# Performance work log

Hardware: AMD Instinct MI355X
Metric: run time of the kernel (lower is better)

Reference implementation:

```python
import jax, jax.numpy as jnp
import numpy as np
from jax import lax

EPS = 1e-8
SLOPE = 0.2

def _modconv(x, wv, W, b, sW, sB, demodulate, pad):
    # StyleGAN2 modulated conv, expressed in the equivalent fused form:
    # scale input by per-sample style s, shared-weight conv, then demodulate output.
    s = wv @ sW.T + sB                                   # [B, Cin]
    y = lax.conv_general_dilated(
        x * s[:, :, None, None], W, (1, 1), [(pad, pad), (pad, pad)],
        dimension_numbers=("NCHW", "OIHW", "NCHW"))      # [B, Cout, H, W]
    if demodulate:
        # d[b,o] = 1/sqrt(sum_{i,k,k} (W[o,i,k,k]*s[b,i])^2 + eps)
        d = lax.rsqrt(jnp.einsum("oihw,bi->bo", W * W, s * s) + EPS)
        y = y * d[:, :, None, None]
    return y + b[None, :, None, None]

def _up2(x):
    B, C, H, W = x.shape
    # matches torch F.interpolate(scale_factor=2, mode='bilinear', align_corners=False)
    return jax.image.resize(x, (B, C, 2 * H, 2 * W), method="bilinear")

def setup_inputs() -> dict:
    B, CIN, COUT, NZ, H = 8, 512, 512, 512, 32
    key = jax.random.key(0)
    ks = jax.random.split(key, 20)
    wscale3 = 1.0 / np.sqrt(CIN * 9)   # kaiming-ish equalized-lr scale baked into weights
    wscale1 = 1.0 / np.sqrt(COUT)
    sscale = 1.0 / np.sqrt(NZ)
    return {
        "maps": jax.random.normal(ks[0], (B, CIN, H, H), jnp.float32),
        "w": jax.random.normal(ks[1], (B, NZ), jnp.float32),
        "rgb": jax.random.normal(ks[2], (B, 3, H, H), jnp.float32),
        "noise0": jax.random.normal(ks[3], (B, 1, 2 * H, 2 * H), jnp.float32),
        "noise1": jax.random.normal(ks[4], (B, 1, 2 * H, 2 * H), jnp.float32),
        "w0": jax.random.normal(ks[5], (COUT, CIN, 3, 3), jnp.float32) * wscale3,
        "b0": jnp.zeros((COUT,), jnp.float32),
        "sW0": jax.random.normal(ks[6], (CIN, NZ), jnp.float32) * sscale,
        "sB0": jnp.ones((CIN,), jnp.float32),
        "ns0": jax.random.normal(ks[7], (COUT,), jnp.float32) * 0.1,
        "w1": jax.random.normal(ks[8], (COUT, COUT, 3, 3), jnp.float32) * wscale3,
        "b1": jnp.zeros((COUT,), jnp.float32),
        "sW1": jax.random.normal(ks[9], (COUT, NZ), jnp.float32) * sscale,
        "sB1": jnp.ones((COUT,), jnp.float32),
        "ns1": jax.random.normal(ks[10], (COUT,), jnp.float32) * 0.1,
        "rgbW": jax.random.normal(ks[11], (3, COUT, 1, 1), jnp.float32) * wscale1,
        "rgbB": jnp.zeros((3,), jnp.float32),
        "rgbSW": jax.random.normal(ks[12], (COUT, NZ), jnp.float32) * sscale,
        "rgbSB": jnp.ones((COUT,), jnp.float32),
    }

def reference(maps, w, rgb, noise0, noise1,
              w0, b0, sW0, sB0, ns0,
              w1, b1, sW1, sB1, ns1,
              rgbW, rgbB, rgbSW, rgbSB):
    rgb = _up2(rgb)
    x = _up2(maps)
    # layer 0: modulated conv 3x3 + noise + leakyrelu
    x = _modconv(x, w, w0, b0, sW0, sB0, True, 1)
    x = x + ns0[None, :, None, None] * noise0
    x = jnp.where(x >= 0, x, SLOPE * x)
    # layer 1
    x = _modconv(x, w, w1, b1, sW1, sB1, True, 1)
    x = x + ns1[None, :, None, None] * noise1
    x = jnp.where(x >= 0, x, SLOPE * x)
    # to_rgb: modulated 1x1 conv, no demodulation
    rgb_out = rgb + _modconv(x, w, rgbW, rgbB, rgbSW, rgbSB, False, 0)
    return (rgb_out, x)
```

## Files before the change

### kernel.cpp

```cpp
#include <hip/hip_runtime.h>

typedef unsigned short u16;
typedef short bf16x8 __attribute__((ext_vector_type(8)));
typedef float f32x4 __attribute__((ext_vector_type(4)));
typedef u16 u16x4 __attribute__((ext_vector_type(4)));
typedef u16 u16x8 __attribute__((ext_vector_type(8)));
typedef unsigned u32x4 __attribute__((ext_vector_type(4)));

__device__ __forceinline__ float b2f(u16 v) {
  union { unsigned u; float f; } x; x.u = ((unsigned)v) << 16; return x.f;
}
__device__ __forceinline__ u16 f2b(float f) {
  unsigned u = __float_as_uint(f);
  unsigned r = (u + 0x7FFFu + ((u >> 16) & 1u)) >> 16;
  return (u16)r;
}
__device__ __forceinline__ float rin(const void* p, size_t i, int bf) {
  return bf ? b2f(((const u16*)p)[i]) : ((const float*)p)[i];
}
__device__ __forceinline__ void async16(const void* g, void* l) {
  __builtin_amdgcn_global_load_lds((const __attribute__((address_space(1))) unsigned*)g,
                                   (__attribute__((address_space(3))) unsigned*)l, 16, 0, 0);
}

__global__ void detect_kernel(const unsigned* __restrict__ w0, int* __restrict__ flag) {
  const int i = threadIdx.x;
  const unsigned lo = w0[i] & 0xFFFFu;
  const unsigned e = (lo >> 7) & 0xFFu;
  const unsigned long long bad = __ballot(e < 100u || e > 126u);
  if (i == 0) flag[0] = (bad == 0ull) ? 1 : 0;
}

__global__ void styleall_kernel(const void* __restrict__ w,
                                const void* __restrict__ sW0, const void* __restrict__ sB0,
                                const void* __restrict__ sW1, const void* __restrict__ sB1,
                                const void* __restrict__ sWR, const void* __restrict__ sBR,
                                float* __restrict__ s0, float* __restrict__ s1,
                                float* __restrict__ sR, const int* __restrict__ flag) {
  const int bf = flag[0];
  const int mat = blockIdx.z, b = blockIdx.y, oc = blockIdx.x;
  const void* sW = (mat == 0) ? sW0 : ((mat == 1) ? sW1 : sWR);
  const void* sB = (mat == 0) ? sB0 : ((mat == 1) ? sB1 : sBR);
  float* out = (mat == 0) ? s0 : ((mat == 1) ? s1 : sR);
  const int tid = threadIdx.x;
  const int i = oc * 64 + (tid >> 2), q = tid & 3;
  float acc = 0.f;
  if (bf) {
    const u16* rp = (const u16*)sW + (size_t)i * 512 + q * 128;
    const u16* wp = (const u16*)w + b * 512 + q * 128;
    for (int z = 0; z < 128; z += 8) {
      u16x8 a = *(const u16x8*)(rp + z), c = *(const u16x8*)(wp + z);
#pragma unroll
      for (int j = 0; j < 8; ++j) acc += b2f(a[j]) * b2f(c[j]);
    }
  } else {
    const float* rp = (const float*)sW + (size_t)i * 512 + q * 128;
    const float* wp = (const float*)w + b * 512 + q * 128;
    for (int z = 0; z < 128; z += 4) {
      f32x4 a = *(const f32x4*)(rp + z), c = *(const f32x4*)(wp + z);
#pragma unroll
      for (int j = 0; j < 4; ++j) acc += a[j] * c[j];
    }
  }
  acc += __shfl_xor(acc, 1, 64);
  acc += __shfl_xor(acc, 2, 64);
  if (q == 0) out[b * 512 + i] = acc + rin(sB, i, bf);
}

__global__ void demod_kernel(const void* __restrict__ W, const float* __restrict__ s,
                             float* __restrict__ d, u16* __restrict__ Wp,
                             const int* __restrict__ flag) {
  const int bf = flag[0];
  const int o = blockIdx.x, tid = threadIdx.x, lane = tid & 63, wv = tid >> 6;
  __shared__ float wsq[512];
  for (int i = tid; i < 512; i += 256) {
    float ss = 0.f;
#pragma unroll
    for (int t = 0; t < 9; ++t) {
      const float f = rin(W, (size_t)(o * 512 + i) * 9 + t, bf);
      ss += f * f;
      Wp[t * 262144 + o * 512 + i] = f2b(f);
    }
    wsq[i] = ss;
  }
  __syncthreads();
#pragma unroll
  for (int bb = 0; bb < 2; ++bb) {
    const int b = wv * 2 + bb;
    float part = 0.f;
    for (int i = lane; i < 512; i += 64) { const float sv = s[b * 512 + i]; part += wsq[i] * sv * sv; }
#pragma unroll
    for (int st = 1; st < 64; st <<= 1) part += __shfl_xor(part, st, 64);
    if (lane == 0) d[b * 512 + o] = rsqrtf(part + 1e-8f);
  }
}

__global__ void upsample_kernel(const void* __restrict__ maps, const float* __restrict__ s,
                                void* __restrict__ outb, int b_base,
                                const int* __restrict__ flag) {
  const int bf = flag[0];
  const size_t esz = bf ? 2 : 4;
  u16* xg = (u16*)((char*)outb + (98304 + (size_t)(b_base >> 2) * 8388608) * esz);
  const int oy = blockIdx.x;
  const int i0 = blockIdx.y * 32;
  const int bl = blockIdx.z;
  const int bg = b_base + bl;
  const int tid = threadIdx.x;
  __shared__ float it[32][2][33];
  const int m = oy >> 1;
  int iy0, iy1; float wy0, wy1;
  if ((oy & 1) == 0) { iy0 = (m > 0) ? m - 1 : 0; iy1 = m; wy0 = 0.25f; wy1 = 0.75f; }
  else               { iy0 = m; iy1 = (m < 31) ? m + 1 : 31; wy0 = 0.75f; wy1 = 0.25f; }
#pragma unroll
  for (int k = 0; k < 8; ++k) {
    const int e = tid + k * 256;
    const int c = e >> 6, wsel = (e >> 5) & 1, x = e & 31;
    const int iy = wsel ? iy1 : iy0;
    it[c][wsel][x] = rin(maps, ((size_t)(bg * 512 + i0 + c) * 32 + iy) * 32 + x, bf);
  }
  __syncthreads();
#pragma unroll
  for (int k = 0; k < 8; ++k) {
    const int e = tid + k * 256;
    const int xx = e >> 5, c = e & 31;
    const int mx = xx >> 1;
    int ix0, ix1; float wx0, wx1;
    if ((xx & 1) == 0) { ix0 = (mx > 0) ? mx - 1 : 0; ix1 = mx; wx0 = 0.25f; wx1 = 0.75f; }
    else               { ix0 = mx; ix1 = (mx < 31) ? mx + 1 : 31; wx0 = 0.75f; wx1 = 0.25f; }
    const float r0 = wx0 * it[c][0][ix0] + wx1 * it[c][0][ix1];
    const float r1 = wx0 * it[c][1][ix0] + wx1 * it[c][1][ix1];
    const float v = (wy0 * r0 + wy1 * r1) * s[bg * 512 + i0 + c];
    xg[((size_t)(bl * 4096) + oy * 64 + xx) * 512 + i0 + c] = f2b(v);
  }
}

__global__ void zero_kernel(u32x4* __restrict__ p, int n16) {
  const int i = blockIdx.x * 256 + threadIdx.x;
  if (i < n16) { u32x4 z = {0, 0, 0, 0}; p[i] = z; }
}

__global__ __launch_bounds__(256) void conv0_kernel(
    const void* __restrict__ outb, const u16* __restrict__ Wp,
    const float* __restrict__ dmod, const void* __restrict__ bias,
    const void* __restrict__ nsc, const void* __restrict__ noise,
    const float* __restrict__ snext, u16* __restrict__ actB,
    const u16* __restrict__ zbuf, int b_base, const int* __restrict__ flag) {
  const int bf = flag[0];
  const size_t esz = bf ? 2 : 4;
  const u16* xg = (const u16*)((const char*)outb + (98304 + (size_t)(b_base >> 2) * 8388608) * esz);
  __shared__ __attribute__((aligned(16))) u16 Alds[8192];
  __shared__ __attribute__((aligned(16))) u16 Blds[8192];
  const int tid = threadIdx.x, lane = tid & 63, w = tid >> 6;
  const int wm = w >> 1, wn = w & 1;
  const int n0 = blockIdx.x * 128, o0 = blockIdx.y * 128;
  const int bl = blockIdx.z, bg = b_base + bl;

  const int srow = w * 32 + (lane >> 2);
  const int scol = (lane & 3) * 8;
  const size_t aA = (size_t)(o0 + srow) * 512 + scol;
  const int p0 = n0 + srow, p1 = p0 + 16;
  const int oy0 = p0 >> 6, ox0 = p0 & 63;
  const int oy1 = p1 >> 6, ox1 = p1 & 63;
  u16* lA0 = &Alds[w * 1024]; u16* lA1 = &Alds[w * 1024 + 512];
  u16* lB0 = &Blds[w * 1024]; u16* lB1 = &Blds[w * 1024 + 512];

  f32x4 acc[4][4] = {};
  const int q = lane >> 4, mrow = lane & 15;

#pragma unroll 1
  for (int t = 0; t < 9; ++t) {
    const int ty = t / 3, tx = t % 3;
    const size_t wbase = (size_t)t * 262144;
    const int iy0 = oy0 + ty - 1, ix0 = ox0 + tx - 1;
    const int iy1 = oy1 + ty - 1, ix1 = ox1 + tx - 1;
    const bool ok0 = ((unsigned)iy0 < 64u) && ((unsigned)ix0 < 64u);
    const bool ok1 = ((unsigned)iy1 < 64u) && ((unsigned)ix1 < 64u);
    const u16* baseB0 = ok0 ? (xg + (((size_t)(bl * 4096) + iy0 * 64 + ix0) * 512 + scol)) : (zbuf + scol);
    const u16* baseB1 = ok1 ? (xg + (((size_t)(bl * 4096) + iy1 * 64 + ix1) * 512 + scol)) : (zbuf + scol);
    const u16* baseA = Wp + wbase + aA;
#pragma unroll 1
    for (int kc = 0; kc < 8; ++kc) {
      const int ko = kc * 64;
      __syncthreads();
      async16(baseA + ko, lA0);
      async16(baseA + ko + 16 * 512, lA1);
      async16(baseA + ko + 32, lA0 + 4096);
      async16(baseA + ko + 32 + 16 * 512, lA1 + 4096);
      async16(baseB0 + ko, lB0);
      async16(baseB1 + ko, lB1);
      async16(baseB0 + ko + 32, lB0 + 4096);
      async16(baseB1 + ko + 32, lB1 + 4096);
      __syncthreads();
#pragma unroll
      for (int kk = 0; kk < 2; ++kk) {
        bf16x8 af[4], bfv[4];
#pragma unroll
        for (int mi = 0; mi < 4; ++mi)
          af[mi] = *(const bf16x8*)&Alds[kk * 4096 + (wm * 64 + mi * 16 + mrow) * 32 + q * 8];
#pragma unroll
        for (int ni = 0; ni < 4; ++ni)
          bfv[ni] = *(const bf16x8*)&Blds[kk * 4096 + (wn * 64 + ni * 16 + mrow) * 32 + q * 8];
#pragma unroll
        for (int mi = 0; mi < 4; ++mi)
#pragma unroll
          for (int ni = 0; ni < 4; ++ni)
            acc[mi][ni] = __builtin_amdgcn_mfma_f32_16x16x32_bf16(af[mi], bfv[ni], acc[mi][ni], 0, 0, 0);
      }
    }
  }

#pragma unroll
  for (int mi = 0; mi < 4; ++mi) {
    const int o = o0 + wm * 64 + mi * 16 + q * 4;
    const f32x4 dv = *(const f32x4*)&dmod[bg * 512 + o];
    const f32x4 sv = *(const f32x4*)&snext[bg * 512 + o];
    float bv[4], nv[4];
#pragma unroll
    for (int r = 0; r < 4; ++r) { bv[r] = rin(bias, o + r, bf); nv[r] = rin(nsc, o + r, bf); }
#pragma unroll
    for (int ni = 0; ni < 4; ++ni) {
      const int p = n0 + wn * 64 + ni * 16 + mrow;
      const float np = rin(noise, (size_t)bg * 4096 + p, bf);
      u16x4 pack;
#pragma unroll
      for (int r = 0; r < 4; ++r) {
        float v = acc[mi][ni][r] * dv[r] + bv[r] + nv[r] * np;
        v = (v >= 0.f) ? v : 0.2f * v;
        pack[r] = f2b(v * sv[r]);
      }
      const int oy = p >> 6, ox = p & 63;
      *(u16x4*)&actB[((size_t)(bl * 4356) + (oy + 1) * 66 + (ox + 1)) * 512 + o] = pack;
    }
  }
}

__global__ __launch_bounds__(256) void conv1_kernel(
    const u16* __restrict__ actB, const u16* __restrict__ Wp,
    const float* __restrict__ dmod, const void* __restrict__ bias,
    const void* __restrict__ nsc, const void* __restrict__ noise,
    const float* __restrict__ sR, const void* __restrict__ rgbW,
    float* __restrict__ rgbacc, void* __restrict__ outb, int b_base,
    const int* __restrict__ flag) {
  const int bf = flag[0];
  __shared__ __attribute__((aligned(16))) u16 Alds[8192];
  __shared__ __attribute__((aligned(16))) u16 Blds[8192];
  __shared__ float rgbWl[1536];
  const int tid = threadIdx.x, lane = tid & 63, w = tid >> 6;
  const int wm = w >> 1, wn = w & 1;
  const int n0 = blockIdx.x * 128, o0 = blockIdx.y * 128;
  const int bl = blockIdx.z, bg = b_base + bl;

  for (int e = tid; e < 1536; e += 256) rgbWl[e] = rin(rgbW, e, bf);

  const int srow = w * 32 + (lane >> 2);
  const int scol = (lane & 3) * 8;
  const size_t aA = (size_t)(o0 + srow) * 512 + scol;
  const int p0 = n0 + srow, p1 = p0 + 16;
  const size_t aB0 = ((size_t)(bl * 4356) + (p0 >> 6) * 66 + (p0 & 63)) * 512 + scol;
  const size_t aB1 = ((size_t)(bl * 4356) + (p1 >> 6) * 66 + (p1 & 63)) * 512 + scol;
  u16* lA0 = &Alds[w * 1024]; u16* lA1 = &Alds[w * 1024 + 512];
  u16* lB0 = &Blds[w * 1024]; u16* lB1 = &Blds[w * 1024 + 512];

  f32x4 acc[4][4] = {};
  const int q = lane >> 4, mrow = lane & 15;

#pragma unroll 1
  for (int t = 0; t < 9; ++t) {
    const int toffB = ((t / 3) * 66 + (t % 3)) * 512;
    const u16* baseA = Wp + (size_t)t * 262144 + aA;
    const u16* baseB0 = actB + aB0 + toffB;
    const u16* baseB1 = actB + aB1 + toffB;
#pragma unroll 1
    for (int kc = 0; kc < 8; ++kc) {
      const int ko = kc * 64;
      __syncthreads();
      async16(baseA + ko, lA0);
      async16(baseA + ko + 16 * 512, lA1);
      async16(baseA + ko + 32, lA0 + 4096);
      async16(baseA + ko + 32 + 16 * 512, lA1 + 4096);
      async16(baseB0 + ko, lB0);
      async16(baseB1 + ko, lB1);
      async16(baseB0 + ko + 32, lB0 + 4096);
      async16(baseB1 + ko + 32, lB1 + 4096);
      __syncthreads();
#pragma unroll
      for (int kk = 0; kk < 2; ++kk) {
        bf16x8 af[4], bfv[4];
#pragma unroll
        for (int mi = 0; mi < 4; ++mi)
          af[mi] = *(const bf16x8*)&Alds[kk * 4096 + (wm * 64 + mi * 16 + mrow) * 32 + q * 8];
#pragma unroll
        for (int ni = 0; ni < 4; ++ni)
          bfv[ni] = *(const bf16x8*)&Blds[kk * 4096 + (wn * 64 + ni * 16 + mrow) * 32 + q * 8];
#pragma unroll
        for (int mi = 0; mi < 4; ++mi)
#pragma unroll
          for (int ni = 0; ni < 4; ++ni)
            acc[mi][ni] = __builtin_amdgcn_mfma_f32_16x16x32_bf16(af[mi], bfv[ni], acc[mi][ni], 0, 0, 0);
      }
    }
  }

  const size_t esz = bf ? 2 : 4;
  char* xreg = (char*)outb + 98304 * esz;
  float racc[4][3] = {};
#pragma unroll
  for (int mi = 0; mi < 4; ++mi) {
    const int o = o0 + wm * 64 + mi * 16 + q * 4;
    const f32x4 dv = *(const f32x4*)&dmod[bg * 512 + o];
    const f32x4 srv = *(const f32x4*)&sR[bg * 512 + o];
    float bv[4], nv[4], w0l[4], w1l[4], w2l[4];
#pragma unroll
    for (int r = 0; r < 4; ++r) {
      bv[r] = rin(bias, o + r, bf); nv[r] = rin(nsc, o + r, bf);
      w0l[r] = rgbWl[o + r]; w1l[r] = rgbWl[512 + o + r]; w2l[r] = rgbWl[1024 + o + r];
    }
#pragma unroll
    for (int ni = 0; ni < 4; ++ni) {
      const int p = n0 + wn * 64 + ni * 16 + mrow;
      const float np = rin(noise, (size_t)bg * 4096 + p, bf);
#pragma unroll
      for (int r = 0; r < 4; ++r) {
        float v = acc[mi][ni][r] * dv[r] + bv[r] + nv[r] * np;
        v = (v >= 0.f) ? v : 0.2f * v;
        const size_t xi = (size_t)(bg * 512 + o + r) * 4096 + p;
        if (bf) ((u16*)xreg)[xi] = f2b(v); else ((float*)xreg)[xi] = v;
        const float xr = v * srv[r];
        racc[ni][0] += w0l[r] * xr;
        racc[ni][1] += w1l[r] * xr;
        racc[ni][2] += w2l[r] * xr;
      }
    }
  }
#pragma unroll
  for (int ni = 0; ni < 4; ++ni) {
    const int p = n0 + wn * 64 + ni * 16 + mrow;
#pragma unroll
    for (int c = 0; c < 3; ++c) {
      float t = racc[ni][c];
      t += __shfl_xor(t, 16, 64);
      t += __shfl_xor(t, 32, 64);
      if (lane < 16) atomicAdd(&rgbacc[(size_t)(bg * 3 + c) * 4096 + p], t);
    }
  }
}

__global__ void rgbfin_kernel(const float* __restrict__ rgbacc, const void* __restrict__ rgbB,
                              const void* __restrict__ rgb, void* __restrict__ outb,
                              const int* __restrict__ flag) {
  const int bf = flag[0];
  const int g = blockIdx.x * 256 + threadIdx.x;
  const int b = g >> 12, p = g & 4095;
  const int oy = p >> 6, ox = p & 63;
  const int m = oy >> 1; int iy0, iy1; float wy0, wy1;
  if ((oy & 1) == 0) { iy0 = (m > 0) ? m - 1 : 0; iy1 = m; wy0 = 0.25f; wy1 = 0.75f; }
  else               { iy0 = m; iy1 = (m < 31) ? m + 1 : 31; wy0 = 0.75f; wy1 = 0.25f; }
  const int mx = ox >> 1; int ix0, ix1; float wx0, wx1;
  if ((ox & 1) == 0) { ix0 = (mx > 0) ? mx - 1 : 0; ix1 = mx; wx0 = 0.25f; wx1 = 0.75f; }
  else               { ix0 = mx; ix1 = (mx < 31) ? mx + 1 : 31; wx0 = 0.75f; wx1 = 0.25f; }
#pragma unroll
  for (int c = 0; c < 3; ++c) {
    const size_t rb = (size_t)(b * 3 + c) * 1024;
    const float up = wy0 * (wx0 * rin(rgb, rb + iy0 * 32 + ix0, bf) + wx1 * rin(rgb, rb + iy0 * 32 + ix1, bf))
                   + wy1 * (wx0 * rin(rgb, rb + iy1 * 32 + ix0, bf) + wx1 * rin(rgb, rb + iy1 * 32 + ix1, bf));
    const float v = up + rin(rgbB, c, bf) + rgbacc[(size_t)(b * 3 + c) * 4096 + p];
    const size_t oi = ((size_t)(b * 3 + c) << 12) + p;
    if (bf) ((u16*)outb)[oi] = f2b(v); else ((float*)outb)[oi] = v;
  }
}


extern "C" void kernel_launch(void* const* d_in, const int* in_sizes, int n_in,
                              void* d_out, int out_size, void* d_ws, size_t ws_size,
                              hipStream_t stream) {
  const void* maps   = d_in[0];
  const void* wlat   = d_in[1];
  const void* rgb    = d_in[2];
  const void* noise0 = d_in[3];
  const void* noise1 = d_in[4];
  const void* w0     = d_in[5];
  const void* b0     = d_in[6];
  const void* sW0    = d_in[7];
  const void* sB0    = d_in[8];
  const void* ns0    = d_in[9];
  const void* w1     = d_in[10];
  const void* b1     = d_in[11];
  const void* sW1    = d_in[12];
  const void* sB1    = d_in[13];
  const void* ns1    = d_in[14];
  const void* rgbW   = d_in[15];
  const void* rgbB   = d_in[16];
  const void* rgbSW  = d_in[17];
  const void* rgbSB  = d_in[18];

  char* ws = (char*)d_ws;
  int*   flg    = (int*)(ws + 0);
  float* s0     = (float*)(ws + 1024);
  float* s1     = (float*)(ws + 17408);
  float* sR     = (float*)(ws + 33792);
  float* dm0    = (float*)(ws + 50176);
  float* dm1    = (float*)(ws + 66560);
  u16*   zbuf   = (u16*)(ws + 82944);
  float* rgbacc = (float*)(ws + 87040);
  u16*   Wp0    = (u16*)(ws + 480256);
  u16*   Wp1    = (u16*)(ws + 5198848);
  u16*   actB   = (u16*)(ws + 9917440);

  const bool full = ws_size >= (size_t)(9917440 + 35684352);
  const int NB = full ? 8 : 4;

  detect_kernel<<<1, 64, 0, stream>>>((const unsigned*)w0, flg);
  styleall_kernel<<<dim3(8, 8, 3), 256, 0, stream>>>(wlat, sW0, sB0, sW1, sB1, rgbSW, rgbSB,
                                                     s0, s1, sR, flg);
  demod_kernel<<<512, 256, 0, stream>>>(w0, s0, dm0, Wp0, flg);
  demod_kernel<<<512, 256, 0, stream>>>(w1, s1, dm1, Wp1, flg);
  zero_kernel<<<98, 256, 0, stream>>>((u32x4*)zbuf, 24832);
  zero_kernel<<<(NB * 1115136 + 8713) / 256 + 1, 256, 0, stream>>>(
      (u32x4*)actB, NB * 278784);

  for (int pass = 0; pass < 8 / NB; ++pass) {
    const int b_base = pass * NB;
    upsample_kernel<<<dim3(64, 16, NB), 256, 0, stream>>>(maps, s0, d_out, b_base, flg);
    conv0_kernel<<<dim3(32, 4, NB), 256, 0, stream>>>(d_out, Wp0, dm0, b0, ns0, noise0, s1,
                                                      actB, zbuf, b_base, flg);
    conv1_kernel<<<dim3(32, 4, NB), 256, 0, stream>>>(actB, Wp1, dm1, b1, ns1, noise1, sR,
                                                      rgbW, rgbacc, d_out, b_base, flg);
  }
  rgbfin_kernel<<<128, 256, 0, stream>>>(rgbacc, rgbB, rgb, d_out, flg);
}
```

Baseline: 516.7 us.

## Inline dtype detection, merge demod launches, zero only padding borders

Removes the separate detect kernel by having every kernel recompute the bf16 flag from w0 into shared memory. The two demod launches are merged into one 2D grid, and each block now stages its weight row in LDS with coalesced vector loads. The full-buffer zero fill of the padded activation buffer is replaced by a prep kernel that zeroes only the one-pixel halo border plus the zero buffer. Together these cut launch count and memory traffic, but they add a small global read and a barrier at the start of every block and rely on conv0 writing every interior pixel.

```diff
diff --git a/kernel.cpp b/kernel.cpp
--- a/kernel.cpp
+++ b/kernel.cpp
@@ -22,13 +22,15 @@
   __builtin_amdgcn_global_load_lds((const __attribute__((address_space(1))) unsigned*)g,
                                    (__attribute__((address_space(3))) unsigned*)l, 16, 0, 0);
 }
-
-__global__ void detect_kernel(const unsigned* __restrict__ w0, int* __restrict__ flag) {
-  const int i = threadIdx.x;
-  const unsigned lo = w0[i] & 0xFFFFu;
-  const unsigned e = (lo >> 7) & 0xFFu;
-  const unsigned long long bad = __ballot(e < 100u || e > 126u);
-  if (i == 0) flag[0] = (bad == 0ull) ? 1 : 0;
+__device__ __forceinline__ int detect_bf(const unsigned* __restrict__ w0raw, int tid, int* shflag) {
+  if (tid < 64) {
+    const unsigned lo = w0raw[tid] & 0xFFFFu;
+    const unsigned e = (lo >> 7) & 0xFFu;
+    const unsigned long long bad = __ballot(e < 100u || e > 126u);
+    if (tid == 0) *shflag = (bad == 0ull) ? 1 : 0;
+  }
+  __syncthreads();
+  return *shflag;
 }
 
 __global__ void styleall_kernel(const void* __restrict__ w,
@@ -36,13 +38,14 @@
                                 const void* __restrict__ sW1, const void* __restrict__ sB1,
                                 const void* __restrict__ sWR, const void* __restrict__ sBR,
                                 float* __restrict__ s0, float* __restrict__ s1,
-                                float* __restrict__ sR, const int* __restrict__ flag) {
-  const int bf = flag[0];
+                                float* __restrict__ sR, const unsigned* __restrict__ w0raw) {
+  __shared__ int shflag;
+  const int tid = threadIdx.x;
+  const int bf = detect_bf(w0raw, tid, &shflag);
   const int mat = blockIdx.z, b = blockIdx.y, oc = blockIdx.x;
   const void* sW = (mat == 0) ? sW0 : ((mat == 1) ? sW1 : sWR);
   const void* sB = (mat == 0) ? sB0 : ((mat == 1) ? sB1 : sBR);
   float* out = (mat == 0) ? s0 : ((mat == 1) ? s1 : sR);
-  const int tid = threadIdx.x;
   const int i = oc * 64 + (tid >> 2), q = tid & 3;
   float acc = 0.f;
   if (bf) {
@@ -67,17 +70,43 @@
   if (q == 0) out[b * 512 + i] = acc + rin(sB, i, bf);
 }
 
-__global__ void demod_kernel(const void* __restrict__ W, const float* __restrict__ s,
-                             float* __restrict__ d, u16* __restrict__ Wp,
-                             const int* __restrict__ flag) {
-  const int bf = flag[0];
-  const int o = blockIdx.x, tid = threadIdx.x, lane = tid & 63, wv = tid >> 6;
+__global__ void demod_kernel(const void* __restrict__ W0, const void* __restrict__ W1,
+                             const float* __restrict__ s0, const float* __restrict__ s1,
+                             float* __restrict__ dm0, float* __restrict__ dm1,
+                             u16* __restrict__ Wp0, u16* __restrict__ Wp1,
+                             const unsigned* __restrict__ w0raw) {
+  __shared__ int shflag;
+  __shared__ float wl[4608];
   __shared__ float wsq[512];
+  const int tid = threadIdx.x, lane = tid & 63, wv = tid >> 6;
+  const int bf = detect_bf(w0raw, tid, &shflag);
+  const int o = blockIdx.x, layer = blockIdx.y;
+  const void* W = layer ? W1 : W0;
+  const float* s = layer ? s1 : s0;
+  float* d = layer ? dm1 : dm0;
+  u16* Wp = layer ? Wp1 : Wp0;
+
+  if (bf) {
+    const u16* src = (const u16*)W + (size_t)o * 4608;
+    for (int e = tid; e < 576; e += 256) {
+      u16x8 v = *(const u16x8*)(src + e * 8);
+#pragma unroll
+      for (int j = 0; j < 8; ++j) wl[e * 8 + j] = b2f(v[j]);
+    }
+  } else {
+    const float* src = (const float*)W + (size_t)o * 4608;
+    for (int e = tid; e < 1152; e += 256) {
+      f32x4 v = *(const f32x4*)(src + e * 4);
+#pragma unroll
+      for (int j = 0; j < 4; ++j) wl[e * 4 + j] = v[j];
+    }
+  }
+  __syncthreads();
   for (int i = tid; i < 512; i += 256) {
     float ss = 0.f;
 #pragma unroll
     for (int t = 0; t < 9; ++t) {
-      const float f = rin(W, (size_t)(o * 512 + i) * 9 + t, bf);
+      const float f = wl[i * 9 + t];
       ss += f * f;
       Wp[t * 262144 + o * 512 + i] = f2b(f);
     }
@@ -95,18 +124,37 @@
   }
 }
 
+__global__ void prep_kernel(u16* __restrict__ actB, u32x4* __restrict__ zr, int NB) {
+  const int id = blockIdx.x, tid = threadIdx.x;
+  if (id < NB * 65) {
+    const int bl = id / 65, sub = id - bl * 65;
+    const int c = sub * 256 + tid;
+    const int px = c >> 6, seg = c & 63;
+    int oy, ox;
+    if (px < 66)       { oy = 0;  ox = px; }
+    else if (px < 132) { oy = 65; ox = px - 66; }
+    else { const int e = px - 132; oy = 1 + (e >> 1); ox = (e & 1) * 65; }
+    u32x4 z = {0, 0, 0, 0};
+    *(u32x4*)&actB[((size_t)(bl * 4356) + oy * 66 + ox) * 512 + seg * 8] = z;
+  } else {
+    const int c = (id - NB * 65) * 256 + tid;
+    if (c < 24832) { u32x4 z = {0, 0, 0, 0}; zr[c] = z; }
+  }
+}
+
 __global__ void upsample_kernel(const void* __restrict__ maps, const float* __restrict__ s,
                                 void* __restrict__ outb, int b_base,
-                                const int* __restrict__ flag) {
-  const int bf = flag[0];
+                                const unsigned* __restrict__ w0raw) {
+  __shared__ int shflag;
+  __shared__ float it[32][2][33];
+  const int tid = threadIdx.x;
+  const int bf = detect_bf(w0raw, tid, &shflag);
   const size_t esz = bf ? 2 : 4;
   u16* xg = (u16*)((char*)outb + (98304 + (size_t)(b_base >> 2) * 8388608) * esz);
   const int oy = blockIdx.x;
   const int i0 = blockIdx.y * 32;
   const int bl = blockIdx.z;
   const int bg = b_base + bl;
-  const int tid = threadIdx.x;
-  __shared__ float it[32][2][33];
   const int m = oy >> 1;
   int iy0, iy1; float wy0, wy1;
   if ((oy & 1) == 0) { iy0 = (m > 0) ? m - 1 : 0; iy1 = m; wy0 = 0.25f; wy1 = 0.75f; }
@@ -134,23 +182,19 @@
   }
 }
 
-__global__ void zero_kernel(u32x4* __restrict__ p, int n16) {
-  const int i = blockIdx.x * 256 + threadIdx.x;
-  if (i < n16) { u32x4 z = {0, 0, 0, 0}; p[i] = z; }
-}
-
 __global__ __launch_bounds__(256) void conv0_kernel(
     const void* __restrict__ outb, const u16* __restrict__ Wp,
     const float* __restrict__ dmod, const void* __restrict__ bias,
     const void* __restrict__ nsc, const void* __restrict__ noise,
     const float* __restrict__ snext, u16* __restrict__ actB,
-    const u16* __restrict__ zbuf, int b_base, const int* __restrict__ flag) {
-  const int bf = flag[0];
+    const u16* __restrict__ zbuf, int b_base, const unsigned* __restrict__ w0raw) {
+  __shared__ __attribute__((aligned(16))) u16 Alds[8192];
+  __shared__ __attribute__((aligned(16))) u16 Blds[8192];
+  __shared__ int shflag;
+  const int tid = threadIdx.x, lane = tid & 63, w = tid >> 6;
+  const int bf = detect_bf(w0raw, tid, &shflag);
   const size_t esz = bf ? 2 : 4;
   const u16* xg = (const u16*)((const char*)outb + (98304 + (size_t)(b_base >> 2) * 8388608) * esz);
-  __shared__ __attribute__((aligned(16))) u16 Alds[8192];
-  __shared__ __attribute__((aligned(16))) u16 Blds[8192];
-  const int tid = threadIdx.x, lane = tid & 63, w = tid >> 6;
   const int wm = w >> 1, wn = w & 1;
   const int n0 = blockIdx.x * 128, o0 = blockIdx.y * 128;
   const int bl = blockIdx.z, bg = b_base + bl;
@@ -240,12 +284,13 @@
     const void* __restrict__ nsc, const void* __restrict__ noise,
     const float* __restrict__ sR, const void* __restrict__ rgbW,
     float* __restrict__ rgbacc, void* __restrict__ outb, int b_base,
-    const int* __restrict__ flag) {
-  const int bf = flag[0];
+    const unsigned* __restrict__ w0raw) {
   __shared__ __attribute__((aligned(16))) u16 Alds[8192];
   __shared__ __attribute__((aligned(16))) u16 Blds[8192];
   __shared__ float rgbWl[1536];
+  __shared__ int shflag;
   const int tid = threadIdx.x, lane = tid & 63, w = tid >> 6;
+  const int bf = detect_bf(w0raw, tid, &shflag);
   const int wm = w >> 1, wn = w & 1;
   const int n0 = blockIdx.x * 128, o0 = blockIdx.y * 128;
   const int bl = blockIdx.z, bg = b_base + bl;
@@ -347,9 +392,11 @@
 
 __global__ void rgbfin_kernel(const float* __restrict__ rgbacc, const void* __restrict__ rgbB,
                               const void* __restrict__ rgb, void* __restrict__ outb,
-                              const int* __restrict__ flag) {
-  const int bf = flag[0];
-  const int g = blockIdx.x * 256 + threadIdx.x;
+                              const unsigned* __restrict__ w0raw) {
+  __shared__ int shflag;
+  const int tid = threadIdx.x;
+  const int bf = detect_bf(w0raw, tid, &shflag);
+  const int g = blockIdx.x * 256 + tid;
   const int b = g >> 12, p = g & 4095;
   const int oy = p >> 6, ox = p & 63;
   const int m = oy >> 1; int iy0, iy1; float wy0, wy1;
@@ -392,9 +439,9 @@
   const void* rgbB   = d_in[16];
   const void* rgbSW  = d_in[17];
   const void* rgbSB  = d_in[18];
+  const unsigned* w0raw = (const unsigned*)w0;
 
   char* ws = (char*)d_ws;
-  int*   flg    = (int*)(ws + 0);
   float* s0     = (float*)(ws + 1024);
   float* s1     = (float*)(ws + 17408);
   float* sR     = (float*)(ws + 33792);
@@ -409,22 +456,18 @@
   const bool full = ws_size >= (size_t)(9917440 + 35684352);
   const int NB = full ? 8 : 4;
 
-  detect_kernel<<<1, 64, 0, stream>>>((const unsigned*)w0, flg);
   styleall_kernel<<<dim3(8, 8, 3), 256, 0, stream>>>(wlat, sW0, sB0, sW1, sB1, rgbSW, rgbSB,
-                                                     s0, s1, sR, flg);
-  demod_kernel<<<512, 256, 0, stream>>>(w0, s0, dm0, Wp0, flg);
-  demod_kernel<<<512, 256, 0, stream>>>(w1, s1, dm1, Wp1, flg);
-  zero_kernel<<<98, 256, 0, stream>>>((u32x4*)zbuf, 24832);
-  zero_kernel<<<(NB * 1115136 + 8713) / 256 + 1, 256, 0, stream>>>(
-      (u32x4*)actB, NB * 278784);
+                                                     s0, s1, sR, w0raw);
+  demod_kernel<<<dim3(512, 2), 256, 0, stream>>>(w0, w1, s0, s1, dm0, dm1, Wp0, Wp1, w0raw);
+  prep_kernel<<<NB * 65 + 97, 256, 0, stream>>>(actB, (u32x4*)zbuf, NB);
 
   for (int pass = 0; pass < 8 / NB; ++pass) {
     const int b_base = pass * NB;
-    upsample_kernel<<<dim3(64, 16, NB), 256, 0, stream>>>(maps, s0, d_out, b_base, flg);
+    upsample_kernel<<<dim3(64, 16, NB), 256, 0, stream>>>(maps, s0, d_out, b_base, w0raw);
     conv0_kernel<<<dim3(32, 4, NB), 256, 0, stream>>>(d_out, Wp0, dm0, b0, ns0, noise0, s1,
-                                                      actB, zbuf, b_base, flg);
+                                                      actB, zbuf, b_base, w0raw);
     conv1_kernel<<<dim3(32, 4, NB), 256, 0, stream>>>(actB, Wp1, dm1, b1, ns1, noise1, sR,
-                                                      rgbW, rgbacc, d_out, b_base, flg);
-  }
-  rgbfin_kernel<<<128, 256, 0, stream>>>(rgbacc, rgbB, rgb, d_out, flg);
-}
+                                                      rgbW, rgbacc, d_out, b_base, w0raw);
+  }
+  rgbfin_kernel<<<128, 256, 0, stream>>>(rgbacc, rgbB, rgb, d_out, w0raw);
+}
```

Measured after the change: 504.1 us. 2.4% less time.
